# Optimization experiments

Measured on AMD Instinct MI355X. Metric: run time of the kernel, lower is better.

Reference implementation:

```python
import jax, jax.numpy as jnp
import numpy as np
from jax import lax

NUM_CLASSES = 5
NUM_TASKS = 20
CONV_CHANS = [(64, 3), (64, 64), (128, 64), (128, 128), (256, 128), (256, 256)]  # (out, in)


def setup_inputs() -> dict:
    key = jax.random.key(0)
    ks = jax.random.split(key, 16)
    B = 512
    x = jax.random.normal(ks[0], (B, 3, 32, 32), dtype=jnp.float32)
    tid = jax.random.randint(ks[1], (B,), 0, NUM_TASKS)
    inp = {"x": x, "tid": tid}
    for i, (oc, ic) in enumerate(CONV_CHANS):
        fan_in = ic * 9
        inp[f"w{i}"] = jax.random.normal(ks[2 + 2 * i], (oc, ic, 3, 3), dtype=jnp.float32) * np.float32((2.0 / fan_in) ** 0.5)
        inp[f"b{i}"] = jnp.zeros((oc,), dtype=jnp.float32)
    inp["cw"] = jax.random.normal(ks[14], (NUM_CLASSES * NUM_TASKS, 4096), dtype=jnp.float32) * np.float32(4096 ** -0.5)
    inp["cb"] = jnp.zeros((NUM_CLASSES * NUM_TASKS,), dtype=jnp.float32)
    return inp


def _conv_relu(x, w, b):
    y = lax.conv_general_dilated(x, w, window_strides=(1, 1), padding='SAME',
                                 dimension_numbers=('NCHW', 'OIHW', 'NCHW'))
    return jax.nn.relu(y + b[None, :, None, None])


def _maxpool2(x):
    return lax.reduce_window(x, -jnp.inf, lax.max, (1, 1, 2, 2), (1, 1, 2, 2), 'VALID')


def _forward(x, tid, ws, bs, cw, cb):
    # VGG cfg [64,64,'M',128,128,'M',256,256,'M']
    h = _conv_relu(x, ws[0], bs[0])
    h = _conv_relu(h, ws[1], bs[1])
    h = _maxpool2(h)
    h = _conv_relu(h, ws[2], bs[2])
    h = _conv_relu(h, ws[3], bs[3])
    h = _maxpool2(h)
    h = _conv_relu(h, ws[4], bs[4])
    h = _conv_relu(h, ws[5], bs[5])
    h = _maxpool2(h)                      # [B, 256, 4, 4]
    feat = h.reshape(h.shape[0], -1)      # [B, 4096], matches torch NCHW flatten
    # Batched task-indexed classifier: gather each sample's 5-row weight block.
    w_sel = cw.reshape(NUM_TASKS, NUM_CLASSES, 4096)[tid]   # [B, 5, 4096]
    b_sel = cb.reshape(NUM_TASKS, NUM_CLASSES)[tid]         # [B, 5]
    return jnp.einsum('bcd,bd->bc', w_sel, feat) + b_sel


def reference(x, tid, w0, b0, w1, b1, w2, b2, w3, b3, w4, b4, w5, b5, cw, cb):
    ws = (w0, w1, w2, w3, w4, w5)
    bs = (b0, b1, b2, b3, b4, b5)
    return _forward(x, tid, ws, bs, cw, cb)
```

## Files before the change

kernel.cpp:

```cpp
#include <hip/hip_runtime.h>


typedef __attribute__((ext_vector_type(8))) short short8;
typedef __attribute__((ext_vector_type(4))) float floatx4;
typedef unsigned int uint;
typedef unsigned short ushort;

__device__ __forceinline__ ushort f2bf(float f) {
    uint u = __float_as_uint(f);
    return (ushort)((u + 0x7fffu + ((u >> 16) & 1u)) >> 16);
}
__device__ __forceinline__ float bf2f(ushort h) {
    return __uint_as_float(((uint)h) << 16);
}

__device__ __forceinline__ void wt_lin_one(
    const float* __restrict__ src, short* __restrict__ dst, int OC, int IC, int o)
{
    int j    = o & 7;
    int lane = (o >> 3) & 63;
    int r    = o >> 9;
    int G16  = OC >> 4;
    int g    = r % G16;  r /= G16;
    int kk   = r % 9;
    int icb  = r / 9;
    int oc = g * 16 + (lane & 15);
    int ic = icb * 32 + (lane >> 4) * 8 + j;
    dst[o] = (short)f2bf(src[((long)oc * IC + ic) * 9 + kk]);
}

__global__ __launch_bounds__(256) void wtransform_all(
    const float* __restrict__ w0, const float* __restrict__ w1,
    const float* __restrict__ w2, const float* __restrict__ w3,
    const float* __restrict__ w4, const float* __restrict__ w5,
    short* __restrict__ dst0, short* __restrict__ dst1, short* __restrict__ dst2,
    short* __restrict__ dst3, short* __restrict__ dst4, short* __restrict__ dst5)
{
    int o = blockIdx.x * 256 + threadIdx.x;
    if (o < 2048) {
        int oc = o >> 5, k = o & 31;
        dst0[o] = (k < 27) ? (short)f2bf(w0[oc * 27 + k]) : (short)0;
        return;
    }
    o -= 2048;
    if (o < 36864)  { wt_lin_one(w1, dst1,  64,  64, o); return; }
    o -= 36864;
    if (o < 73728)  { wt_lin_one(w2, dst2, 128,  64, o); return; }
    o -= 73728;
    if (o < 147456) { wt_lin_one(w3, dst3, 128, 128, o); return; }
    o -= 147456;
    if (o < 294912) { wt_lin_one(w4, dst4, 256, 128, o); return; }
    o -= 294912;
    if (o < 589824) { wt_lin_one(w5, dst5, 256, 256, o); return; }
}

__global__ __launch_bounds__(256, 2) void conv0_mfma(
    const float* __restrict__ x, const short* __restrict__ wT0,
    const float* __restrict__ b0, ushort* __restrict__ out)
{
    __shared__ float  s_x[3 * 18 * 34];
    __shared__ ushort s_b[4 * 512 * 8];

    const int tid  = threadIdx.x;
    const int wv   = tid >> 6;
    const int lane = tid & 63;
    const int quad = lane >> 4;
    const int l16  = lane & 15;
    const int b    = blockIdx.x >> 1;
    const int r0   = (blockIdx.x & 1) * 16;

    for (int idx = tid; idx < 3 * 18 * 34; idx += 256) {
        int c   = idx / 612;
        int rem = idx - c * 612;
        int ry  = rem / 34, rx = rem - ry * 34;
        int gy  = r0 + ry - 1, gx = rx - 1;
        float v = 0.f;
        if (gy >= 0 && gy < 32 && gx >= 0 && gx < 32)
            v = x[(((long)b * 3 + c) * 32 + gy) * 32 + gx];
        s_x[idx] = v;
    }
    __syncthreads();

#pragma unroll
    for (int rep = 0; rep < 2; ++rep) {
        int pxl = rep * 256 + tid;
        int py = pxl >> 5, px = pxl & 31;
        ushort v[32];
#pragma unroll
        for (int c = 0; c < 3; ++c)
#pragma unroll
            for (int ky = 0; ky < 3; ++ky)
#pragma unroll
                for (int kx = 0; kx < 3; ++kx)
                    v[c * 9 + ky * 3 + kx] = f2bf(s_x[c * 612 + (py + ky) * 34 + (px + kx)]);
#pragma unroll
        for (int k = 27; k < 32; ++k) v[k] = 0;
#pragma unroll
        for (int q = 0; q < 4; ++q)
            *(uint4*)(&s_b[(q * 512 + pxl) * 8]) = *(const uint4*)(v + q * 8);
    }
    __syncthreads();

    floatx4 acc[4][8];
#pragma unroll
    for (int i = 0; i < 4; ++i)
#pragma unroll
        for (int t = 0; t < 8; ++t) acc[i][t] = (floatx4)0.f;

    short8 afr[4];
#pragma unroll
    for (int i = 0; i < 4; ++i)
        afr[i] = *(const short8*)(wT0 + (i * 16 + l16) * 32 + quad * 8);
#pragma unroll
    for (int t = 0; t < 8; ++t) {
        int pxl = wv * 128 + t * 16 + l16;
        short8 bfr = *(const short8*)(&s_b[(quad * 512 + pxl) * 8]);
#pragma unroll
        for (int i = 0; i < 4; ++i)
            acc[i][t] = __builtin_amdgcn_mfma_f32_16x16x32_bf16(afr[i], bfr, acc[i][t], 0, 0, 0);
    }

#pragma unroll
    for (int i = 0; i < 4; ++i) {
        int oc0 = i * 16 + quad * 4;
        float4 bv = *(const float4*)(b0 + oc0);
#pragma unroll
        for (int t = 0; t < 8; ++t) {
            int pxl = wv * 128 + t * 16 + l16;
            int py = pxl >> 5, px = pxl & 31;
            long dst = ((((long)b * 8 + (oc0 >> 3)) * 32 + r0 + py) * 32 + px) * 8 + (oc0 & 7);
            float v0 = acc[i][t][0] + bv.x;
            float v1 = acc[i][t][1] + bv.y;
            float v2 = acc[i][t][2] + bv.z;
            float v3 = acc[i][t][3] + bv.w;
            ushort o[4];
            o[0] = f2bf(v0 > 0.f ? v0 : 0.f);
            o[1] = f2bf(v1 > 0.f ? v1 : 0.f);
            o[2] = f2bf(v2 > 0.f ? v2 : 0.f);
            o[3] = f2bf(v3 > 0.f ? v3 : 0.f);
            *(uint2*)(out + dst) = *(uint2*)o;
        }
    }
}

template<int IC, int OC, int H, int W, int ROWS, int OCGROUPS, int OCSPLIT,
         int NSTAGE, bool POOL>
__global__ __launch_bounds__(256, 4) void conv_so(
    const ushort* __restrict__ act_in,
    const short*  __restrict__ wTs,
    const float*  __restrict__ bias,
    ushort* __restrict__ act_out)
{
    constexpr int PXG   = 4 / OCGROUPS;
    constexpr int NFRAG = (ROWS * W) / (PXG * 16);
    constexpr int OCBLK = OCGROUPS * 64;
    constexpr int WPAD  = W + 2;
    constexpr int RPAD  = ROWS + 2;
    constexpr int UNITS = RPAD * WPAD;
    constexpr int SEGS  = H / ROWS;
    constexpr int C8I   = IC / 8;
    constexpr int C8H   = C8I / NSTAGE;
    constexpr int CPUP  = C8H + 1;
    constexpr int G16   = OC / 16;
    constexpr int NICBH = (IC / 32) / NSTAGE;
    constexpr int C8O   = OC / 8;
    constexpr int TMAX  = (IC / 32) * 9;
    constexpr int PSTR  = OCBLK + 8;
    constexpr int SHW   = UNITS * CPUP * 8;
    constexpr int PHW   = POOL ? ROWS * W * PSTR : 0;
    constexpr int LDSHW = SHW > PHW ? SHW : PHW;

    __shared__ ushort s_act[LDSHW];

    const int tid  = threadIdx.x;
    const int wv   = tid >> 6;
    const int lane = tid & 63;
    const int quad = lane >> 4;
    const int l16  = lane & 15;

    int bx = blockIdx.x;
    const int ocb = bx % OCSPLIT;  bx /= OCSPLIT;
    const int seg = bx % SEGS;
    const int b   = bx / SEGS;
    const int r0  = seg * ROWS;
    const int ocg = wv % OCGROUPS;
    const int pxg = wv / OCGROUPS;
    const int gbase = ocb * OCGROUPS * 4 + ocg * 4;

    floatx4 acc[4][NFRAG];
#pragma unroll
    for (int i = 0; i < 4; ++i)
#pragma unroll
        for (int t = 0; t < NFRAG; ++t) acc[i][t] = (floatx4)0.f;

    int bbase[NFRAG];
#pragma unroll
    for (int t = 0; t < NFRAG; ++t) {
        int pxl = pxg * (NFRAG * 16) + t * 16 + l16;
        int py  = pxl / W, px = pxl - py * W;
        bbase[t] = (py * WPAD + px) * CPUP * 8;
    }

    const short8* wb = (const short8*)wTs;
    short8 afr[4];
#pragma unroll
    for (int i = 0; i < 4; ++i)
        afr[i] = wb[((long)0 * G16 + gbase + i) * 64 + lane];

    int tl = 0;
    for (int st = 0; st < NSTAGE; ++st) {
        if (st) __syncthreads();
        for (int c = tid; c < UNITS * C8H; c += 256) {
            int sub  = c / UNITS;
            int unit = c - sub * UNITS;
            int ry   = unit / WPAD, cx = unit - ry * WPAD;
            int gy   = r0 + ry - 1, gx = cx - 1;
            uint4 val = make_uint4(0, 0, 0, 0);
            if ((unsigned)gy < (unsigned)H && (unsigned)gx < (unsigned)W) {
                long src = ((((long)b * C8I + st * C8H + sub) * H + gy) * W + gx) * 8;
                val = *(const uint4*)(act_in + src);
            }
            *(uint4*)(&s_act[((size_t)unit * CPUP + sub) * 8]) = val;
        }
        __syncthreads();

        for (int icb = 0; icb < NICBH; ++icb) {
#pragma unroll
            for (int kk = 0; kk < 9; ++kk) {
                const int ky = kk / 3, kx = kk - ky * 3;
                const int koff = ((ky * WPAD + kx) * CPUP + icb * 4 + quad) * 8;
                short8 bfr[NFRAG];
#pragma unroll
                for (int t = 0; t < NFRAG; ++t)
                    bfr[t] = *(const short8*)(&s_act[bbase[t] + koff]);
                int tn = (tl + 1 < TMAX) ? tl + 1 : tl;
                short8 afrN[4];
#pragma unroll
                for (int i = 0; i < 4; ++i)
                    afrN[i] = wb[((long)tn * G16 + gbase + i) * 64 + lane];
#pragma unroll
                for (int i = 0; i < 4; ++i)
#pragma unroll
                    for (int t = 0; t < NFRAG; ++t)
                        acc[i][t] = __builtin_amdgcn_mfma_f32_16x16x32_bf16(
                            afr[i], bfr[t], acc[i][t], 0, 0, 0);
#pragma unroll
                for (int i = 0; i < 4; ++i) afr[i] = afrN[i];
                ++tl;
            }
        }
    }

    if constexpr (!POOL) {
#pragma unroll
        for (int i = 0; i < 4; ++i) {
            int oc0 = ocb * OCBLK + ocg * 64 + i * 16 + quad * 4;
            float4 bv = *(const float4*)(bias + oc0);
#pragma unroll
            for (int t = 0; t < NFRAG; ++t) {
                int pxl = pxg * (NFRAG * 16) + t * 16 + l16;
                int py  = pxl / W, px = pxl - py * W;
                long dst = ((((long)b * C8O + (oc0 >> 3)) * H + r0 + py) * W + px) * 8 + (oc0 & 7);
                float v0 = acc[i][t][0] + bv.x;
                float v1 = acc[i][t][1] + bv.y;
                float v2 = acc[i][t][2] + bv.z;
                float v3 = acc[i][t][3] + bv.w;
                ushort o[4];
                o[0] = f2bf(v0 > 0.f ? v0 : 0.f);
                o[1] = f2bf(v1 > 0.f ? v1 : 0.f);
                o[2] = f2bf(v2 > 0.f ? v2 : 0.f);
                o[3] = f2bf(v3 > 0.f ? v3 : 0.f);
                *(uint2*)(act_out + dst) = *(uint2*)o;
            }
        }
    } else {
        __syncthreads();
        ushort* s_pool = s_act;
#pragma unroll
        for (int i = 0; i < 4; ++i) {
            int ocl = ocg * 64 + i * 16 + quad * 4;
            float4 bv = *(const float4*)(bias + ocb * OCBLK + ocl);
#pragma unroll
            for (int t = 0; t < NFRAG; ++t) {
                int pxl = pxg * (NFRAG * 16) + t * 16 + l16;
                float v0 = acc[i][t][0] + bv.x;
                float v1 = acc[i][t][1] + bv.y;
                float v2 = acc[i][t][2] + bv.z;
                float v3 = acc[i][t][3] + bv.w;
                ushort o[4];
                o[0] = f2bf(v0 > 0.f ? v0 : 0.f);
                o[1] = f2bf(v1 > 0.f ? v1 : 0.f);
                o[2] = f2bf(v2 > 0.f ? v2 : 0.f);
                o[3] = f2bf(v3 > 0.f ? v3 : 0.f);
                *(uint2*)(&s_pool[pxl * PSTR + ocl]) = *(uint2*)o;
            }
        }
        __syncthreads();
        constexpr int PH = ROWS / 2, PW = W / 2, HOT = H / 2, C8B = OCBLK / 8;
        const int pr0 = r0 / 2;
        for (int u = tid; u < PH * PW * C8B; u += 256) {
            int c8 = u % C8B;
            int pp = u / C8B;
            int xo = pp % PW, yo = pp / PW;
            const ushort* p00 = &s_pool[((2 * yo) * W + 2 * xo) * PSTR + c8 * 8];
            uint4 q0 = *(const uint4*)(p00);
            uint4 q1 = *(const uint4*)(p00 + PSTR);
            uint4 q2 = *(const uint4*)(p00 + W * PSTR);
            uint4 q3 = *(const uint4*)(p00 + W * PSTR + PSTR);
            const ushort* a0 = (const ushort*)&q0;
            const ushort* a1 = (const ushort*)&q1;
            const ushort* a2 = (const ushort*)&q2;
            const ushort* a3 = (const ushort*)&q3;
            ushort r[8];
#pragma unroll
            for (int j = 0; j < 8; ++j) {
                ushort m0 = a0[j] > a1[j] ? a0[j] : a1[j];
                ushort m1 = a2[j] > a3[j] ? a2[j] : a3[j];
                r[j] = m0 > m1 ? m0 : m1;
            }
            long dst = ((((long)b * C8O + ocb * C8B + c8) * HOT + pr0 + yo) * PW + xo) * 8;
            *(uint4*)(act_out + dst) = *(uint4*)r;
        }
    }
}

__global__ __launch_bounds__(256) void classifier_k(
    const ushort* __restrict__ feat, const int* __restrict__ tids,
    const float* __restrict__ cw, const float* __restrict__ cb,
    float* __restrict__ out, int B)
{
    int g = blockIdx.x * 256 + threadIdx.x;
    int wid = g >> 6, lane = g & 63;
    if (wid >= B * 5) return;
    int b = wid / 5, c = wid - b * 5;
    int t = tids[b];
    const float* wrow = cw + (long)(t * 5 + c) * 4096;
    const ushort* f = feat + (long)b * 4096;
    float s = 0.f;
#pragma unroll 4
    for (int d = lane; d < 4096; d += 64) {
        int fidx = (((d >> 7) * 16) + (d & 15)) * 8 + ((d >> 4) & 7);
        s += wrow[d] * bf2f(f[fidx]);
    }
#pragma unroll
    for (int off = 32; off > 0; off >>= 1) s += __shfl_down(s, off, 64);
    if (lane == 0) out[wid] = s + cb[t * 5 + c];
}

extern "C" void kernel_launch(void* const* d_in, const int* in_sizes, int n_in,
                              void* d_out, int out_size, void* d_ws, size_t ws_size,
                              hipStream_t stream)
{
    const float* x   = (const float*)d_in[0];
    const int*   tid = (const int*)d_in[1];
    const float* w0 = (const float*)d_in[2];  const float* b0 = (const float*)d_in[3];
    const float* w1 = (const float*)d_in[4];  const float* b1 = (const float*)d_in[5];
    const float* w2 = (const float*)d_in[6];  const float* b2 = (const float*)d_in[7];
    const float* w3 = (const float*)d_in[8];  const float* b3 = (const float*)d_in[9];
    const float* w4 = (const float*)d_in[10]; const float* b4 = (const float*)d_in[11];
    const float* w5 = (const float*)d_in[12]; const float* b5 = (const float*)d_in[13];
    const float* cw = (const float*)d_in[14];
    const float* cb = (const float*)d_in[15];
    float* outp = (float*)d_out;

    const int B = in_sizes[0] / (3 * 32 * 32);

    short* wt0  = (short*)d_ws;
    short* wts1 = wt0 + 2048;
    short* wts2 = wts1 + 36864;
    short* wts3 = wts2 + 73728;
    short* wts4 = wts3 + 147456;
    short* wts5 = wts4 + 294912;
    const size_t WT_HW = 2048 + 36864 + 73728 + 147456 + 294912 + 589824;
    const size_t fixed_bytes = WT_HW * 2;

    int Bc = B;
    while (Bc > 2 && fixed_bytes + (size_t)Bc * 2 * 65536 * 2 > ws_size) Bc >>= 1;
    if (Bc < 2) Bc = 2;

    ushort* bufA = (ushort*)((short*)d_ws + WT_HW);
    ushort* bufB = bufA + (size_t)Bc * 65536;

    wtransform_all<<<(int)((WT_HW + 255) / 256), 256, 0, stream>>>(
        w0, w1, w2, w3, w4, w5, wt0, wts1, wts2, wts3, wts4, wts5);

    for (int cb0 = 0; cb0 < B; cb0 += Bc) {
        const float* xc = x + (size_t)cb0 * 3 * 32 * 32;
        const int* tidc = tid + cb0;
        float* outc = outp + (size_t)cb0 * 5;

        conv0_mfma<<<Bc * 2, 256, 0, stream>>>(xc, wt0, b0, bufA);
        conv_so<64, 64, 32, 32, 8, 1, 1, 2, true><<<Bc * 4, 256, 0, stream>>>(bufA, wts1, b1, bufB);
        conv_so<64, 128, 16, 16, 8, 2, 1, 1, false><<<Bc * 2, 256, 0, stream>>>(bufB, wts2, b2, bufA);
        conv_so<128, 128, 16, 16, 8, 2, 1, 2, true><<<Bc * 2, 256, 0, stream>>>(bufA, wts3, b3, bufB);
        conv_so<128, 256, 8, 8, 8, 2, 2, 1, false><<<Bc * 2, 256, 0, stream>>>(bufB, wts4, b4, bufA);
        conv_so<256, 256, 8, 8, 8, 2, 2, 2, true><<<Bc * 2, 256, 0, stream>>>(bufA, wts5, b5, bufB);
        classifier_k<<<(Bc * 5 * 64 + 255) / 256, 256, 0, stream>>>(bufB, tidc, cw, cb, outc, Bc);
    }
}
```

Measured before the change: 322.4 us.

## Enlarge conv tiles to eight fragments per wave, batch samples, pool via shuffles

The conv kernel now always gives each wave eight 16-pixel fragments, using taller row tiles or several samples per block, so every weight fragment fed to the MFMAs is reused across more pixels. The fused 2x2 max-pool no longer stages results through LDS; it does the pooling with cross-lane shuffles in registers and then stores directly. The blocks are larger, fewer blocks are launched, and launch bounds drop to 2 waves per SIMD. This cuts weight-load traffic and the LDS round trip plus barriers in the pool epilogue, but raises register pressure and lowers occupancy.

Measured after the change: 348.1 us. 1.08x slower.

```diff
diff --git a/kernel.cpp b/kernel.cpp
--- a/kernel.cpp
+++ b/kernel.cpp
@@ -143,20 +143,48 @@
     }
 }
 
+__device__ __forceinline__ floatx4 relu_bias(floatx4 a, float4 bv) {
+    floatx4 r;
+    r[0] = a[0] + bv.x; r[1] = a[1] + bv.y; r[2] = a[2] + bv.z; r[3] = a[3] + bv.w;
+#pragma unroll
+    for (int j = 0; j < 4; ++j) r[j] = r[j] > 0.f ? r[j] : 0.f;
+    return r;
+}
+__device__ __forceinline__ floatx4 max_xor(floatx4 v, int m) {
+    floatx4 r;
+#pragma unroll
+    for (int j = 0; j < 4; ++j) {
+        float o = __shfl_xor(v[j], m, 64);
+        r[j] = v[j] > o ? v[j] : o;
+    }
+    return r;
+}
+__device__ __forceinline__ floatx4 max4(floatx4 a, floatx4 b) {
+    floatx4 r;
+#pragma unroll
+    for (int j = 0; j < 4; ++j) r[j] = a[j] > b[j] ? a[j] : b[j];
+    return r;
+}
+__device__ __forceinline__ void store_bf4(ushort* p, floatx4 v) {
+    ushort o[4];
+#pragma unroll
+    for (int j = 0; j < 4; ++j) o[j] = f2bf(v[j]);
+    *(uint2*)p = *(uint2*)o;
+}
+
 template<int IC, int OC, int H, int W, int ROWS, int OCGROUPS, int OCSPLIT,
-         int NSTAGE, bool POOL>
-__global__ __launch_bounds__(256, 4) void conv_so(
+         int NSAMP, int NSTAGE, bool POOL>
+__global__ __launch_bounds__(256, 2) void conv_nf8(
     const ushort* __restrict__ act_in,
     const short*  __restrict__ wTs,
     const float*  __restrict__ bias,
     ushort* __restrict__ act_out)
 {
     constexpr int PXG   = 4 / OCGROUPS;
-    constexpr int NFRAG = (ROWS * W) / (PXG * 16);
-    constexpr int OCBLK = OCGROUPS * 64;
     constexpr int WPAD  = W + 2;
     constexpr int RPAD  = ROWS + 2;
-    constexpr int UNITS = RPAD * WPAD;
+    constexpr int SUNIT = RPAD * WPAD;
+    constexpr int UNITS = NSAMP * SUNIT;
     constexpr int SEGS  = H / ROWS;
     constexpr int C8I   = IC / 8;
     constexpr int C8H   = C8I / NSTAGE;
@@ -165,12 +193,10 @@
     constexpr int NICBH = (IC / 32) / NSTAGE;
     constexpr int C8O   = OC / 8;
     constexpr int TMAX  = (IC / 32) * 9;
-    constexpr int PSTR  = OCBLK + 8;
-    constexpr int SHW   = UNITS * CPUP * 8;
-    constexpr int PHW   = POOL ? ROWS * W * PSTR : 0;
-    constexpr int LDSHW = SHW > PHW ? SHW : PHW;
-
-    __shared__ ushort s_act[LDSHW];
+    static_assert(PXG * 128 == NSAMP * ROWS * W, "px tiling mismatch");
+    static_assert(!POOL || W != 8 || PXG == 1, "W=8 pool needs PXG=1");
+
+    __shared__ ushort s_act[UNITS * CPUP * 8];
 
     const int tid  = threadIdx.x;
     const int wv   = tid >> 6;
@@ -181,24 +207,26 @@
     int bx = blockIdx.x;
     const int ocb = bx % OCSPLIT;  bx /= OCSPLIT;
     const int seg = bx % SEGS;
-    const int b   = bx / SEGS;
+    const int b0  = (bx / SEGS) * NSAMP;
     const int r0  = seg * ROWS;
     const int ocg = wv % OCGROUPS;
     const int pxg = wv / OCGROUPS;
-    const int gbase = ocb * OCGROUPS * 4 + ocg * 4;
-
-    floatx4 acc[4][NFRAG];
+    const int gbase = (ocb * OCGROUPS + ocg) * 4;
+
+    floatx4 acc[4][8];
 #pragma unroll
     for (int i = 0; i < 4; ++i)
 #pragma unroll
-        for (int t = 0; t < NFRAG; ++t) acc[i][t] = (floatx4)0.f;
-
-    int bbase[NFRAG];
-#pragma unroll
-    for (int t = 0; t < NFRAG; ++t) {
-        int pxl = pxg * (NFRAG * 16) + t * 16 + l16;
-        int py  = pxl / W, px = pxl - py * W;
-        bbase[t] = (py * WPAD + px) * CPUP * 8;
+        for (int t = 0; t < 8; ++t) acc[i][t] = (floatx4)0.f;
+
+    int bbase[8];
+#pragma unroll
+    for (int t = 0; t < 8; ++t) {
+        int pxl = pxg * 128 + t * 16 + l16;
+        int s   = pxl / (ROWS * W);
+        int p2  = pxl - s * (ROWS * W);
+        int py  = p2 / W, px = p2 - py * W;
+        bbase[t] = (s * SUNIT + py * WPAD + px) * CPUP * 8;
     }
 
     const short8* wb = (const short8*)wTs;
@@ -213,11 +241,13 @@
         for (int c = tid; c < UNITS * C8H; c += 256) {
             int sub  = c / UNITS;
             int unit = c - sub * UNITS;
-            int ry   = unit / WPAD, cx = unit - ry * WPAD;
+            int s    = unit / SUNIT;
+            int rem  = unit - s * SUNIT;
+            int ry   = rem / WPAD, cx = rem - ry * WPAD;
             int gy   = r0 + ry - 1, gx = cx - 1;
             uint4 val = make_uint4(0, 0, 0, 0);
             if ((unsigned)gy < (unsigned)H && (unsigned)gx < (unsigned)W) {
-                long src = ((((long)b * C8I + st * C8H + sub) * H + gy) * W + gx) * 8;
+                long src = ((((long)(b0 + s) * C8I + st * C8H + sub) * H + gy) * W + gx) * 8;
                 val = *(const uint4*)(act_in + src);
             }
             *(uint4*)(&s_act[((size_t)unit * CPUP + sub) * 8]) = val;
@@ -229,9 +259,9 @@
             for (int kk = 0; kk < 9; ++kk) {
                 const int ky = kk / 3, kx = kk - ky * 3;
                 const int koff = ((ky * WPAD + kx) * CPUP + icb * 4 + quad) * 8;
-                short8 bfr[NFRAG];
-#pragma unroll
-                for (int t = 0; t < NFRAG; ++t)
+                short8 bfr[8];
+#pragma unroll
+                for (int t = 0; t < 8; ++t)
                     bfr[t] = *(const short8*)(&s_act[bbase[t] + koff]);
                 int tn = (tl + 1 < TMAX) ? tl + 1 : tl;
                 short8 afrN[4];
@@ -241,7 +271,7 @@
 #pragma unroll
                 for (int i = 0; i < 4; ++i)
 #pragma unroll
-                    for (int t = 0; t < NFRAG; ++t)
+                    for (int t = 0; t < 8; ++t)
                         acc[i][t] = __builtin_amdgcn_mfma_f32_16x16x32_bf16(
                             afr[i], bfr[t], acc[i][t], 0, 0, 0);
 #pragma unroll
@@ -251,75 +281,65 @@
         }
     }
 
-    if constexpr (!POOL) {
-#pragma unroll
-        for (int i = 0; i < 4; ++i) {
-            int oc0 = ocb * OCBLK + ocg * 64 + i * 16 + quad * 4;
-            float4 bv = *(const float4*)(bias + oc0);
-#pragma unroll
-            for (int t = 0; t < NFRAG; ++t) {
-                int pxl = pxg * (NFRAG * 16) + t * 16 + l16;
-                int py  = pxl / W, px = pxl - py * W;
-                long dst = ((((long)b * C8O + (oc0 >> 3)) * H + r0 + py) * W + px) * 8 + (oc0 & 7);
-                float v0 = acc[i][t][0] + bv.x;
-                float v1 = acc[i][t][1] + bv.y;
-                float v2 = acc[i][t][2] + bv.z;
-                float v3 = acc[i][t][3] + bv.w;
-                ushort o[4];
-                o[0] = f2bf(v0 > 0.f ? v0 : 0.f);
-                o[1] = f2bf(v1 > 0.f ? v1 : 0.f);
-                o[2] = f2bf(v2 > 0.f ? v2 : 0.f);
-                o[3] = f2bf(v3 > 0.f ? v3 : 0.f);
-                *(uint2*)(act_out + dst) = *(uint2*)o;
+#pragma unroll
+    for (int i = 0; i < 4; ++i) {
+        const int oc0 = (gbase + i) * 16 + quad * 4;
+        const float4 bv = *(const float4*)(bias + oc0);
+        if constexpr (!POOL) {
+#pragma unroll
+            for (int t = 0; t < 8; ++t) {
+                int pxl = pxg * 128 + t * 16 + l16;
+                int s   = pxl / (ROWS * W);
+                int p2  = pxl - s * (ROWS * W);
+                int py  = p2 / W, px = p2 - py * W;
+                long dst = ((((long)(b0 + s) * C8O + (oc0 >> 3)) * H + r0 + py) * W + px) * 8 + (oc0 & 7);
+                store_bf4(act_out + dst, relu_bias(acc[i][t], bv));
             }
-        }
-    } else {
-        __syncthreads();
-        ushort* s_pool = s_act;
-#pragma unroll
-        for (int i = 0; i < 4; ++i) {
-            int ocl = ocg * 64 + i * 16 + quad * 4;
-            float4 bv = *(const float4*)(bias + ocb * OCBLK + ocl);
-#pragma unroll
-            for (int t = 0; t < NFRAG; ++t) {
-                int pxl = pxg * (NFRAG * 16) + t * 16 + l16;
-                float v0 = acc[i][t][0] + bv.x;
-                float v1 = acc[i][t][1] + bv.y;
-                float v2 = acc[i][t][2] + bv.z;
-                float v3 = acc[i][t][3] + bv.w;
-                ushort o[4];
-                o[0] = f2bf(v0 > 0.f ? v0 : 0.f);
-                o[1] = f2bf(v1 > 0.f ? v1 : 0.f);
-                o[2] = f2bf(v2 > 0.f ? v2 : 0.f);
-                o[3] = f2bf(v3 > 0.f ? v3 : 0.f);
-                *(uint2*)(&s_pool[pxl * PSTR + ocl]) = *(uint2*)o;
+        } else {
+            floatx4 r[8];
+#pragma unroll
+            for (int t = 0; t < 8; ++t)
+                r[t] = max_xor(relu_bias(acc[i][t], bv), 1);
+            if constexpr (W == 16) {
+                constexpr int HO = H / 2, WO = W / 2;
+#pragma unroll
+                for (int tp = 0; tp < 4; ++tp) {
+                    floatx4 m = max4(r[2 * tp], r[2 * tp + 1]);
+                    if ((l16 & 1) == 0) {
+                        int prow = pxg * 4 + tp;
+                        int pcol = l16 >> 1;
+                        long dst = ((((long)b0 * C8O + (oc0 >> 3)) * HO + prow) * WO + pcol) * 8 + (oc0 & 7);
+                        store_bf4(act_out + dst, m);
+                    }
+                }
+            } else if constexpr (W == 32) {
+                constexpr int HO = H / 2, WO = W / 2;
+#pragma unroll
+                for (int j = 0; j < 2; ++j)
+#pragma unroll
+                    for (int k = 0; k < 2; ++k) {
+                        floatx4 m = max4(r[j * 4 + k], r[j * 4 + k + 2]);
+                        if ((l16 & 1) == 0) {
+                            int prow = r0 / 2 + pxg * 2 + j;
+                            int pcol = k * 8 + (l16 >> 1);
+                            long dst = ((((long)b0 * C8O + (oc0 >> 3)) * HO + prow) * WO + pcol) * 8 + (oc0 & 7);
+                            store_bf4(act_out + dst, m);
+                        }
+                    }
+            } else {
+                constexpr int HO = H / 2, WO = W / 2;
+#pragma unroll
+                for (int t = 0; t < 8; ++t) {
+                    floatx4 m = max_xor(r[t], 8);
+                    if ((l16 & 1) == 0 && l16 < 8) {
+                        int bb   = b0 + (t >> 2);
+                        int prow = t & 3;
+                        int pcol = l16 >> 1;
+                        long dst = ((((long)bb * C8O + (oc0 >> 3)) * HO + prow) * WO + pcol) * 8 + (oc0 & 7);
+                        store_bf4(act_out + dst, m);
+                    }
+                }
             }
-        }
-        __syncthreads();
-        constexpr int PH = ROWS / 2, PW = W / 2, HOT = H / 2, C8B = OCBLK / 8;
-        const int pr0 = r0 / 2;
-        for (int u = tid; u < PH * PW * C8B; u += 256) {
-            int c8 = u % C8B;
-            int pp = u / C8B;
-            int xo = pp % PW, yo = pp / PW;
-            const ushort* p00 = &s_pool[((2 * yo) * W + 2 * xo) * PSTR + c8 * 8];
-            uint4 q0 = *(const uint4*)(p00);
-            uint4 q1 = *(const uint4*)(p00 + PSTR);
-            uint4 q2 = *(const uint4*)(p00 + W * PSTR);
-            uint4 q3 = *(const uint4*)(p00 + W * PSTR + PSTR);
-            const ushort* a0 = (const ushort*)&q0;
-            const ushort* a1 = (const ushort*)&q1;
-            const ushort* a2 = (const ushort*)&q2;
-            const ushort* a3 = (const ushort*)&q3;
-            ushort r[8];
-#pragma unroll
-            for (int j = 0; j < 8; ++j) {
-                ushort m0 = a0[j] > a1[j] ? a0[j] : a1[j];
-                ushort m1 = a2[j] > a3[j] ? a2[j] : a3[j];
-                r[j] = m0 > m1 ? m0 : m1;
-            }
-            long dst = ((((long)b * C8O + ocb * C8B + c8) * HOT + pr0 + yo) * PW + xo) * 8;
-            *(uint4*)(act_out + dst) = *(uint4*)r;
         }
     }
 }
@@ -390,11 +410,11 @@
         float* outc = outp + (size_t)cb0 * 5;
 
         conv0_mfma<<<Bc * 2, 256, 0, stream>>>(xc, wt0, b0, bufA);
-        conv_so<64, 64, 32, 32, 8, 1, 1, 2, true><<<Bc * 4, 256, 0, stream>>>(bufA, wts1, b1, bufB);
-        conv_so<64, 128, 16, 16, 8, 2, 1, 1, false><<<Bc * 2, 256, 0, stream>>>(bufB, wts2, b2, bufA);
-        conv_so<128, 128, 16, 16, 8, 2, 1, 2, true><<<Bc * 2, 256, 0, stream>>>(bufA, wts3, b3, bufB);
-        conv_so<128, 256, 8, 8, 8, 2, 2, 1, false><<<Bc * 2, 256, 0, stream>>>(bufB, wts4, b4, bufA);
-        conv_so<256, 256, 8, 8, 8, 2, 2, 2, true><<<Bc * 2, 256, 0, stream>>>(bufA, wts5, b5, bufB);
+        conv_nf8<64, 64, 32, 32, 16, 1, 1, 1, 2, true><<<Bc * 2, 256, 0, stream>>>(bufA, wts1, b1, bufB);
+        conv_nf8<64, 128, 16, 16, 16, 2, 1, 1, 1, false><<<Bc, 256, 0, stream>>>(bufB, wts2, b2, bufA);
+        conv_nf8<128, 128, 16, 16, 16, 2, 1, 1, 2, true><<<Bc, 256, 0, stream>>>(bufA, wts3, b3, bufB);
+        conv_nf8<128, 256, 8, 8, 8, 4, 1, 2, 2, false><<<Bc / 2, 256, 0, stream>>>(bufB, wts4, b4, bufA);
+        conv_nf8<256, 256, 8, 8, 8, 4, 1, 2, 2, true><<<Bc / 2, 256, 0, stream>>>(bufA, wts5, b5, bufB);
         classifier_k<<<(Bc * 5 * 64 + 255) / 256, 256, 0, stream>>>(bufB, tidc, cw, cb, outc, Bc);
     }
 }
```
